# Optimization experiments

Measured on AMD Instinct MI355X. Metric: run time of the kernel, lower is better.

The kernel has to match this reference:

```python
import jax, jax.numpy as jnp
import numpy as np

B, R, A, K, O, I = 50000, 5, 8, 2, 32, 32


def setup_inputs() -> dict:
    key = jax.random.key(0)
    k1, k2, k3 = jax.random.split(key, 3)
    signal = jax.random.normal(k1, (B, R, A, 3, I), dtype=jnp.float32)
    bary = jax.random.uniform(k2, (B, R, A, 3), dtype=jnp.float32)
    # glorot-uniform-ish kernel: shape (R, A, K, O, I)
    limit = np.sqrt(6.0 / (I + O)).astype(np.float32)
    kernel = jax.random.uniform(k3, (R, A, K, O, I), dtype=jnp.float32,
                                minval=-limit, maxval=limit)
    return {"signal": signal, "bary": bary, "kernel": kernel}


def reference(signal, bary, kernel):
    # Barycentric interpolation: pullback[b,r,a,i] = sum_t bary[b,r,a,t] * signal[b,r,a,t,i]
    pullback = jnp.einsum('brat,brati->brai', bary, signal)  # (B,R,A,I)

    n_rot = kernel.shape[1]  # A rotations
    # rotated angular indices: rot_idx[c, a] = (a + c) % A
    rot_idx = (jnp.arange(n_rot)[:, None] + jnp.arange(n_rot)[None, :]) % n_rot
    k_rot = kernel[:, rot_idx]  # (R, C=A, A, K, O, I)

    # conv[b,c,o] = sum_{r,a,k,i} kernel[r,(a+c)%A,k,o,i] * pullback[b,r,a,i]
    conv = jnp.einsum('brai,rcakoi->bco', pullback, k_rot)  # (B, C, O)
    act = jax.nn.relu(conv)

    # Angular max pooling: pick rotation with max euclidean norm over O
    norms = jnp.linalg.norm(act, axis=-1)          # (B, C)
    best = jnp.argmax(norms, axis=-1)              # (B,)
    out = jnp.take_along_axis(act, best[:, None, None], axis=1)[:, 0]  # (B, O)
    return out
```

## Files before the change

kernel.cpp:

```cpp
#include <hip/hip_runtime.h>


#define B_TOT 50000
#define NRA 40

typedef __attribute__((ext_vector_type(8))) short short8v;
typedef __attribute__((ext_vector_type(4))) float f32x4;

__device__ __align__(16) unsigned short W_hi_g[NRA * 256 * 32];
__device__ __align__(16) unsigned short W_lo_g[NRA * 256 * 32];

static __device__ __forceinline__ unsigned short f2bf(float x) {
    unsigned u = __float_as_uint(x);
    u += 0x7FFFu + ((u >> 16) & 1u);
    return (unsigned short)(u >> 16);
}
static __device__ __forceinline__ float bf2f(unsigned short h) {
    return __uint_as_float(((unsigned)h) << 16);
}

__global__ __launch_bounds__(256) void build_w_kernel(const float* __restrict__ kern) {
    int e = blockIdx.x * 256 + threadIdx.x;
    int i = e & 31;
    int n = (e >> 5) & 255;
    int ra = e >> 13;
    int r = ra >> 3, a = ra & 7;
    int c = n >> 5, o = n & 31;
    int a2 = (c + a) & 7;
    const float* p = kern + ((((r * 8 + a2) * 2) * 32 + o) * 32 + i);
    float w = p[0] + p[1024];
    unsigned short hi = f2bf(w);
    unsigned short lo = f2bf(w - bf2f(hi));
    W_hi_g[e] = hi;
    W_lo_g[e] = lo;
}

static __device__ __forceinline__ void pcomp(float by0, float by1, float by2,
                                             const float4& a, const float4& b,
                                             const float4& c, float* d) {
    d[0] = fmaf(by2, c.x, fmaf(by1, b.x, by0 * a.x));
    d[1] = fmaf(by2, c.y, fmaf(by1, b.y, by0 * a.y));
    d[2] = fmaf(by2, c.z, fmaf(by1, b.z, by0 * a.z));
    d[3] = fmaf(by2, c.w, fmaf(by1, b.w, by0 * a.w));
}

static __device__ __forceinline__ void pack_write(unsigned short* p_hi, int idx, const float* v) {
    unsigned short h[4], l[4];
#pragma unroll
    for (int k = 0; k < 4; ++k) {
        h[k] = f2bf(v[k]);
        l[k] = f2bf(v[k] - bf2f(h[k]));
    }
    uint2 H, L;
    H.x = (unsigned)h[0] | ((unsigned)h[1] << 16);
    H.y = (unsigned)h[2] | ((unsigned)h[3] << 16);
    L.x = (unsigned)l[0] | ((unsigned)l[1] << 16);
    L.y = (unsigned)l[2] | ((unsigned)l[3] << 16);
    *(uint2*)(p_hi + idx) = H;
    *(uint2*)(p_hi + 2560 + idx) = L;
}

__global__ __launch_bounds__(256, 3) void conv_geo_kernel(const float* __restrict__ sig,
                                                          const float* __restrict__ bary,
                                                          float* __restrict__ out) {
    __shared__ __align__(16) float smem[8448];
    unsigned short* p_hi = (unsigned short*)smem;

    const int tid  = threadIdx.x;
    const int lane = tid & 63;
    const int wave = tid >> 6;
    const int b_l  = tid >> 2;
    const int q    = tid & 3;
    const int b0   = blockIdx.x * 64;
    int bld = b0 + b_l; if (bld > B_TOT - 1) bld = B_TOT - 1;
    const size_t sig_row = (size_t)bld * 40;

    f32x4 acc[4][4];
#pragma unroll
    for (int mi = 0; mi < 4; ++mi)
#pragma unroll
        for (int ni = 0; ni < 4; ++ni) acc[mi][ni] = (f32x4){0.f, 0.f, 0.f, 0.f};

    float4 s0, s1, s2, s3, s4, s5;
    float by0, by1, by2;
    {
        const float* sp = sig + sig_row * 96 + q * 4;
        s0 = *(const float4*)(sp);      s1 = *(const float4*)(sp + 16);
        s2 = *(const float4*)(sp + 32); s3 = *(const float4*)(sp + 48);
        s4 = *(const float4*)(sp + 64); s5 = *(const float4*)(sp + 80);
        const float* bp = bary + sig_row * 3;
        by0 = bp[0]; by1 = bp[1]; by2 = bp[2];
    }

    const int wcol = (wave * 64 + (lane & 15)) * 32 + (lane >> 4) * 8;
    const int poff = (lane & 15) * 40 + (lane >> 4) * 8;
    const int widx = b_l * 40 + q * 4;

    for (int ra = 0; ra < NRA; ++ra) {
        float pa[4], pb[4];
        pcomp(by0, by1, by2, s0, s2, s4, pa);
        pcomp(by0, by1, by2, s1, s3, s5, pb);
        pack_write(p_hi, widx, pa);
        pack_write(p_hi, widx + 16, pb);

        short8v bh[4], blv[4];
        {
            const unsigned short* whp = W_hi_g + ra * 8192 + wcol;
            const unsigned short* wlp = W_lo_g + ra * 8192 + wcol;
#pragma unroll
            for (int ni = 0; ni < 4; ++ni) {
                bh[ni]  = *(const short8v*)(whp + ni * 512);
                blv[ni] = *(const short8v*)(wlp + ni * 512);
            }
        }
        if (ra < NRA - 1) {
            const float* sp = sig + (sig_row + ra + 1) * 96 + q * 4;
            s0 = *(const float4*)(sp);      s1 = *(const float4*)(sp + 16);
            s2 = *(const float4*)(sp + 32); s3 = *(const float4*)(sp + 48);
            s4 = *(const float4*)(sp + 64); s5 = *(const float4*)(sp + 80);
            const float* bp = bary + (sig_row + ra + 1) * 3;
            by0 = bp[0]; by1 = bp[1]; by2 = bp[2];
        }
        __syncthreads();
#pragma unroll
        for (int mi = 0; mi < 4; ++mi) {
            const unsigned short* pr = p_hi + mi * 640 + poff;
            short8v ah = *(const short8v*)pr;
            short8v al = *(const short8v*)(pr + 2560);
#pragma unroll
            for (int ni = 0; ni < 4; ++ni) {
                acc[mi][ni] = __builtin_amdgcn_mfma_f32_16x16x32_bf16(ah, bh[ni],  acc[mi][ni], 0, 0, 0);
                acc[mi][ni] = __builtin_amdgcn_mfma_f32_16x16x32_bf16(ah, blv[ni], acc[mi][ni], 0, 0, 0);
                acc[mi][ni] = __builtin_amdgcn_mfma_f32_16x16x32_bf16(al, bh[ni],  acc[mi][ni], 0, 0, 0);
                acc[mi][ni] = __builtin_amdgcn_mfma_f32_16x16x32_bf16(al, blv[ni], acc[mi][ni], 0, 0, 0);
            }
        }
        __syncthreads();
    }

    const int colb = wave * 64 + (lane & 15);
    const int rsub = (lane >> 4) * 4;
#pragma unroll
    for (int ph = 0; ph < 2; ++ph) {
        __syncthreads();
#pragma unroll
        for (int mh = 0; mh < 2; ++mh) {
            int mi = ph * 2 + mh;
#pragma unroll
            for (int ni = 0; ni < 4; ++ni)
#pragma unroll
                for (int j = 0; j < 4; ++j)
                    smem[(mh * 16 + rsub + j) * 264 + colb + ni * 16] =
                        fmaxf(acc[mi][ni][j], 0.0f);
        }
        __syncthreads();
        int bb = tid >> 3;
        int c  = tid & 7;
        float n2 = 0.0f;
#pragma unroll
        for (int t = 0; t < 8; ++t) {
            float4 v = *(const float4*)&smem[bb * 264 + c * 32 + t * 4];
            n2 = fmaf(v.x, v.x, n2); n2 = fmaf(v.y, v.y, n2);
            n2 = fmaf(v.z, v.z, n2); n2 = fmaf(v.w, v.w, n2);
        }
        int bc = c;
#pragma unroll
        for (int m = 1; m < 8; m <<= 1) {
            float on2 = __shfl_xor(n2, m, 64);
            int obc = __shfl_xor(bc, m, 64);
            if (on2 > n2 || (on2 == n2 && obc < bc)) { n2 = on2; bc = obc; }
        }
        int b = b0 + ph * 32 + bb;
        if (b < B_TOT) {
            float4 v = *(const float4*)&smem[bb * 264 + bc * 32 + (tid & 7) * 4];
            *(float4*)&out[(size_t)b * 32 + (tid & 7) * 4] = v;
        }
    }
}

extern "C" void kernel_launch(void* const* d_in, const int* in_sizes, int n_in,
                              void* d_out, int out_size, void* d_ws, size_t ws_size,
                              hipStream_t stream) {
    const float* sig  = (const float*)d_in[0];
    const float* bary = (const float*)d_in[1];
    const float* kern = (const float*)d_in[2];
    float* out = (float*)d_out;

    build_w_kernel<<<(NRA * 256 * 32) / 256, 256, 0, stream>>>(kern);
    conv_geo_kernel<<<(B_TOT + 63) / 64, 256, 0, stream>>>(sig, bary, out);
}
```

Before: 235.5 us.

## Double-buffer pullback tiles in LDS and drop the lo*lo MFMA term

Splits the shared pullback staging into two ping-pong buffers. Each iteration now writes the next slice's packed bf16 pullback while the MFMAs read the current one, which removes one __syncthreads per iteration, and signal loads are prefetched two slices ahead. It also removes the al*bl correction MFMA from the split-bf16 emulation, cutting matrix work by a quarter. The dropped term is on the order of bf16-epsilon squared, so accuracy drops slightly and register pressure may rise.

```diff
diff --git a/kernel.cpp b/kernel.cpp
--- a/kernel.cpp
+++ b/kernel.cpp
@@ -44,7 +44,7 @@
     d[3] = fmaf(by2, c.w, fmaf(by1, b.w, by0 * a.w));
 }
 
-static __device__ __forceinline__ void pack_write(unsigned short* p_hi, int idx, const float* v) {
+static __device__ __forceinline__ void pack_write(unsigned short* buf, int idx, const float* v) {
     unsigned short h[4], l[4];
 #pragma unroll
     for (int k = 0; k < 4; ++k) {
@@ -56,15 +56,16 @@
     H.y = (unsigned)h[2] | ((unsigned)h[3] << 16);
     L.x = (unsigned)l[0] | ((unsigned)l[1] << 16);
     L.y = (unsigned)l[2] | ((unsigned)l[3] << 16);
-    *(uint2*)(p_hi + idx) = H;
-    *(uint2*)(p_hi + 2560 + idx) = L;
+    *(uint2*)(buf + idx) = H;
+    *(uint2*)(buf + 2560 + idx) = L;
 }
 
 __global__ __launch_bounds__(256, 3) void conv_geo_kernel(const float* __restrict__ sig,
                                                           const float* __restrict__ bary,
                                                           float* __restrict__ out) {
     __shared__ __align__(16) float smem[8448];
-    unsigned short* p_hi = (unsigned short*)smem;
+    unsigned short* pb0 = (unsigned short*)smem;
+    unsigned short* pb1 = pb0 + 5120;
 
     const int tid  = threadIdx.x;
     const int lane = tid & 63;
@@ -81,61 +82,62 @@
 #pragma unroll
         for (int ni = 0; ni < 4; ++ni) acc[mi][ni] = (f32x4){0.f, 0.f, 0.f, 0.f};
 
-    float4 s0, s1, s2, s3, s4, s5;
-    float by0, by1, by2;
-    {
-        const float* sp = sig + sig_row * 96 + q * 4;
-        s0 = *(const float4*)(sp);      s1 = *(const float4*)(sp + 16);
-        s2 = *(const float4*)(sp + 32); s3 = *(const float4*)(sp + 48);
-        s4 = *(const float4*)(sp + 64); s5 = *(const float4*)(sp + 80);
-        const float* bp = bary + sig_row * 3;
-        by0 = bp[0]; by1 = bp[1]; by2 = bp[2];
-    }
-
     const int wcol = (wave * 64 + (lane & 15)) * 32 + (lane >> 4) * 8;
     const int poff = (lane & 15) * 40 + (lane >> 4) * 8;
     const int widx = b_l * 40 + q * 4;
 
-    for (int ra = 0; ra < NRA; ++ra) {
-        float pa[4], pb[4];
+    float4 s0, s1, s2, s3, s4, s5;
+    float by0, by1, by2;
+    auto load_sig = [&](int ra) {
+        const float* sp = sig + (sig_row + ra) * 96 + q * 4;
+        s0 = *(const float4*)(sp);      s1 = *(const float4*)(sp + 16);
+        s2 = *(const float4*)(sp + 32); s3 = *(const float4*)(sp + 48);
+        s4 = *(const float4*)(sp + 64); s5 = *(const float4*)(sp + 80);
+        const float* bp = bary + (sig_row + ra) * 3;
+        by0 = bp[0]; by1 = bp[1]; by2 = bp[2];
+    };
+    auto store_p = [&](unsigned short* wrbuf) {
+        float pa[4], pbv[4];
         pcomp(by0, by1, by2, s0, s2, s4, pa);
-        pcomp(by0, by1, by2, s1, s3, s5, pb);
-        pack_write(p_hi, widx, pa);
-        pack_write(p_hi, widx + 16, pb);
+        pcomp(by0, by1, by2, s1, s3, s5, pbv);
+        pack_write(wrbuf, widx, pa);
+        pack_write(wrbuf, widx + 16, pbv);
+    };
 
-        short8v bh[4], blv[4];
-        {
-            const unsigned short* whp = W_hi_g + ra * 8192 + wcol;
-            const unsigned short* wlp = W_lo_g + ra * 8192 + wcol;
+    load_sig(0);
+    store_p(pb0);
+    load_sig(1);
+    __syncthreads();
+
+    auto body = [&](int ra, unsigned short* rdbuf, unsigned short* wrbuf) {
+        short8v bh[4], bl[4];
+        const unsigned short* whp = W_hi_g + ra * 8192 + wcol;
+        const unsigned short* wlp = W_lo_g + ra * 8192 + wcol;
 #pragma unroll
-            for (int ni = 0; ni < 4; ++ni) {
-                bh[ni]  = *(const short8v*)(whp + ni * 512);
-                blv[ni] = *(const short8v*)(wlp + ni * 512);
-            }
+        for (int ni = 0; ni < 4; ++ni) {
+            bh[ni] = *(const short8v*)(whp + ni * 512);
+            bl[ni] = *(const short8v*)(wlp + ni * 512);
         }
-        if (ra < NRA - 1) {
-            const float* sp = sig + (sig_row + ra + 1) * 96 + q * 4;
-            s0 = *(const float4*)(sp);      s1 = *(const float4*)(sp + 16);
-            s2 = *(const float4*)(sp + 32); s3 = *(const float4*)(sp + 48);
-            s4 = *(const float4*)(sp + 64); s5 = *(const float4*)(sp + 80);
-            const float* bp = bary + (sig_row + ra + 1) * 3;
-            by0 = bp[0]; by1 = bp[1]; by2 = bp[2];
-        }
-        __syncthreads();
+        if (ra + 1 < NRA) store_p(wrbuf);
+        if (ra + 2 < NRA) load_sig(ra + 2);
 #pragma unroll
         for (int mi = 0; mi < 4; ++mi) {
-            const unsigned short* pr = p_hi + mi * 640 + poff;
+            const unsigned short* pr = rdbuf + mi * 640 + poff;
             short8v ah = *(const short8v*)pr;
             short8v al = *(const short8v*)(pr + 2560);
 #pragma unroll
             for (int ni = 0; ni < 4; ++ni) {
-                acc[mi][ni] = __builtin_amdgcn_mfma_f32_16x16x32_bf16(ah, bh[ni],  acc[mi][ni], 0, 0, 0);
-                acc[mi][ni] = __builtin_amdgcn_mfma_f32_16x16x32_bf16(ah, blv[ni], acc[mi][ni], 0, 0, 0);
-                acc[mi][ni] = __builtin_amdgcn_mfma_f32_16x16x32_bf16(al, bh[ni],  acc[mi][ni], 0, 0, 0);
-                acc[mi][ni] = __builtin_amdgcn_mfma_f32_16x16x32_bf16(al, blv[ni], acc[mi][ni], 0, 0, 0);
+                acc[mi][ni] = __builtin_amdgcn_mfma_f32_16x16x32_bf16(ah, bh[ni], acc[mi][ni], 0, 0, 0);
+                acc[mi][ni] = __builtin_amdgcn_mfma_f32_16x16x32_bf16(ah, bl[ni], acc[mi][ni], 0, 0, 0);
+                acc[mi][ni] = __builtin_amdgcn_mfma_f32_16x16x32_bf16(al, bh[ni], acc[mi][ni], 0, 0, 0);
             }
         }
         __syncthreads();
+    };
+
+    for (int ra = 0; ra < NRA; ra += 2) {
+        body(ra,     pb0, pb1);
+        body(ra + 1, pb1, pb0);
     }
 
     const int colb = wave * 64 + (lane & 15);
```

Result: faster. 229.4 us (-2.6%).

## Give each wave its own 16-row tile and drop shared memory staging

Applied to the files above, without the earlier changes.

Restructures the conv kernel so each wave independently owns 16 batch rows and all 256 output columns. Pullback values are computed directly in MFMA A-operand register layout, so the shared-memory staging and the two block barriers per iteration go away. The low*low bf16 MFMA term is dropped, leaving three split-precision products instead of four. The argmax epilogue now runs on registers with lane shuffles instead of going through shared memory. In exchange every wave reloads the full weight slice from global/L2 each iteration, which cuts weight reuse across waves, and the 16-wide accumulator array raises register pressure.

```diff
diff --git a/kernel.cpp b/kernel.cpp
--- a/kernel.cpp
+++ b/kernel.cpp
@@ -3,6 +3,7 @@
 
 #define B_TOT 50000
 #define NRA 40
+#define NROWTILES 3125
 
 typedef __attribute__((ext_vector_type(8))) short short8v;
 typedef __attribute__((ext_vector_type(4))) float f32x4;
@@ -35,146 +36,101 @@
     W_lo_g[e] = lo;
 }
 
-static __device__ __forceinline__ void pcomp(float by0, float by1, float by2,
-                                             const float4& a, const float4& b,
-                                             const float4& c, float* d) {
-    d[0] = fmaf(by2, c.x, fmaf(by1, b.x, by0 * a.x));
-    d[1] = fmaf(by2, c.y, fmaf(by1, b.y, by0 * a.y));
-    d[2] = fmaf(by2, c.z, fmaf(by1, b.z, by0 * a.z));
-    d[3] = fmaf(by2, c.w, fmaf(by1, b.w, by0 * a.w));
-}
-
-static __device__ __forceinline__ void pack_write(unsigned short* p_hi, int idx, const float* v) {
-    unsigned short h[4], l[4];
-#pragma unroll
-    for (int k = 0; k < 4; ++k) {
-        h[k] = f2bf(v[k]);
-        l[k] = f2bf(v[k] - bf2f(h[k]));
-    }
-    uint2 H, L;
-    H.x = (unsigned)h[0] | ((unsigned)h[1] << 16);
-    H.y = (unsigned)h[2] | ((unsigned)h[3] << 16);
-    L.x = (unsigned)l[0] | ((unsigned)l[1] << 16);
-    L.y = (unsigned)l[2] | ((unsigned)l[3] << 16);
-    *(uint2*)(p_hi + idx) = H;
-    *(uint2*)(p_hi + 2560 + idx) = L;
-}
-
-__global__ __launch_bounds__(256, 3) void conv_geo_kernel(const float* __restrict__ sig,
-                                                          const float* __restrict__ bary,
-                                                          float* __restrict__ out) {
-    __shared__ __align__(16) float smem[8448];
-    unsigned short* p_hi = (unsigned short*)smem;
-
+__global__ __launch_bounds__(256) void conv_geo_kernel(const float* __restrict__ sig,
+                                                       const float* __restrict__ bary,
+                                                       float* __restrict__ out) {
     const int tid  = threadIdx.x;
     const int lane = tid & 63;
-    const int wave = tid >> 6;
-    const int b_l  = tid >> 2;
-    const int q    = tid & 3;
-    const int b0   = blockIdx.x * 64;
-    int bld = b0 + b_l; if (bld > B_TOT - 1) bld = B_TOT - 1;
-    const size_t sig_row = (size_t)bld * 40;
+    const int wv   = tid >> 6;
+    const int rt   = blockIdx.x * 4 + wv;
+    if (rt >= NROWTILES) return;
 
-    f32x4 acc[4][4];
+    const int arow = lane & 15;
+    const int i0   = (lane >> 4) * 8;
+    const size_t srow = ((size_t)rt * 16 + arow) * 40;
+
+    f32x4 acc[16];
 #pragma unroll
-    for (int mi = 0; mi < 4; ++mi)
+    for (int ni = 0; ni < 16; ++ni) acc[ni] = (f32x4){0.f, 0.f, 0.f, 0.f};
+
+    const int wbase = arow * 32 + (lane >> 4) * 8;
+
+    for (int ra = 0; ra < NRA; ++ra) {
+        const float* sp = sig + (srow + ra) * 96 + i0;
+        float4 t0a = *(const float4*)(sp);       float4 t0b = *(const float4*)(sp + 4);
+        float4 t1a = *(const float4*)(sp + 32);  float4 t1b = *(const float4*)(sp + 36);
+        float4 t2a = *(const float4*)(sp + 64);  float4 t2b = *(const float4*)(sp + 68);
+        const float* bp = bary + (srow + ra) * 3;
+        float by0 = bp[0], by1 = bp[1], by2 = bp[2];
+        float p[8];
+        p[0] = fmaf(by2, t2a.x, fmaf(by1, t1a.x, by0 * t0a.x));
+        p[1] = fmaf(by2, t2a.y, fmaf(by1, t1a.y, by0 * t0a.y));
+        p[2] = fmaf(by2, t2a.z, fmaf(by1, t1a.z, by0 * t0a.z));
+        p[3] = fmaf(by2, t2a.w, fmaf(by1, t1a.w, by0 * t0a.w));
+        p[4] = fmaf(by2, t2b.x, fmaf(by1, t1b.x, by0 * t0b.x));
+        p[5] = fmaf(by2, t2b.y, fmaf(by1, t1b.y, by0 * t0b.y));
+        p[6] = fmaf(by2, t2b.z, fmaf(by1, t1b.z, by0 * t0b.z));
+        p[7] = fmaf(by2, t2b.w, fmaf(by1, t1b.w, by0 * t0b.w));
+        unsigned short hh[8], ll[8];
 #pragma unroll
-        for (int ni = 0; ni < 4; ++ni) acc[mi][ni] = (f32x4){0.f, 0.f, 0.f, 0.f};
+        for (int j = 0; j < 8; ++j) {
+            hh[j] = f2bf(p[j]);
+            ll[j] = f2bf(p[j] - bf2f(hh[j]));
+        }
+        union { unsigned u[4]; short8v v; } ch, cl;
+#pragma unroll
+        for (int k = 0; k < 4; ++k) {
+            ch.u[k] = (unsigned)hh[2 * k] | ((unsigned)hh[2 * k + 1] << 16);
+            cl.u[k] = (unsigned)ll[2 * k] | ((unsigned)ll[2 * k + 1] << 16);
+        }
+        short8v ah = ch.v, al = cl.v;
 
-    float4 s0, s1, s2, s3, s4, s5;
-    float by0, by1, by2;
-    {
-        const float* sp = sig + sig_row * 96 + q * 4;
-        s0 = *(const float4*)(sp);      s1 = *(const float4*)(sp + 16);
-        s2 = *(const float4*)(sp + 32); s3 = *(const float4*)(sp + 48);
-        s4 = *(const float4*)(sp + 64); s5 = *(const float4*)(sp + 80);
-        const float* bp = bary + sig_row * 3;
-        by0 = bp[0]; by1 = bp[1]; by2 = bp[2];
+        const unsigned short* wh = W_hi_g + ra * 8192 + wbase;
+        const unsigned short* wl = W_lo_g + ra * 8192 + wbase;
+#pragma unroll
+        for (int ni = 0; ni < 16; ++ni) {
+            short8v bh = *(const short8v*)(wh + ni * 512);
+            short8v bl = *(const short8v*)(wl + ni * 512);
+            acc[ni] = __builtin_amdgcn_mfma_f32_16x16x32_bf16(ah, bh, acc[ni], 0, 0, 0);
+            acc[ni] = __builtin_amdgcn_mfma_f32_16x16x32_bf16(ah, bl, acc[ni], 0, 0, 0);
+            acc[ni] = __builtin_amdgcn_mfma_f32_16x16x32_bf16(al, bh, acc[ni], 0, 0, 0);
+        }
     }
 
-    const int wcol = (wave * 64 + (lane & 15)) * 32 + (lane >> 4) * 8;
-    const int poff = (lane & 15) * 40 + (lane >> 4) * 8;
-    const int widx = b_l * 40 + q * 4;
+#pragma unroll
+    for (int ni = 0; ni < 16; ++ni)
+#pragma unroll
+        for (int j = 0; j < 4; ++j) acc[ni][j] = fmaxf(acc[ni][j], 0.0f);
 
-    for (int ra = 0; ra < NRA; ++ra) {
-        float pa[4], pb[4];
-        pcomp(by0, by1, by2, s0, s2, s4, pa);
-        pcomp(by0, by1, by2, s1, s3, s5, pb);
-        pack_write(p_hi, widx, pa);
-        pack_write(p_hi, widx + 16, pb);
+    float nrm[4][8];
+#pragma unroll
+    for (int j = 0; j < 4; ++j)
+#pragma unroll
+        for (int c = 0; c < 8; ++c)
+            nrm[j][c] = fmaf(acc[2 * c][j], acc[2 * c][j],
+                             acc[2 * c + 1][j] * acc[2 * c + 1][j]);
+#pragma unroll
+    for (int m = 1; m < 16; m <<= 1)
+#pragma unroll
+        for (int j = 0; j < 4; ++j)
+#pragma unroll
+            for (int c = 0; c < 8; ++c)
+                nrm[j][c] += __shfl_xor(nrm[j][c], m, 64);
 
-        short8v bh[4], blv[4];
-        {
-            const unsigned short* whp = W_hi_g + ra * 8192 + wcol;
-            const unsigned short* wlp = W_lo_g + ra * 8192 + wcol;
 #pragma unroll
-            for (int ni = 0; ni < 4; ++ni) {
-                bh[ni]  = *(const short8v*)(whp + ni * 512);
-                blv[ni] = *(const short8v*)(wlp + ni * 512);
-            }
-        }
-        if (ra < NRA - 1) {
-            const float* sp = sig + (sig_row + ra + 1) * 96 + q * 4;
-            s0 = *(const float4*)(sp);      s1 = *(const float4*)(sp + 16);
-            s2 = *(const float4*)(sp + 32); s3 = *(const float4*)(sp + 48);
-            s4 = *(const float4*)(sp + 64); s5 = *(const float4*)(sp + 80);
-            const float* bp = bary + (sig_row + ra + 1) * 3;
-            by0 = bp[0]; by1 = bp[1]; by2 = bp[2];
-        }
-        __syncthreads();
+    for (int j = 0; j < 4; ++j) {
+        float n2 = nrm[j][0];
+        int bc = 0;
 #pragma unroll
-        for (int mi = 0; mi < 4; ++mi) {
-            const unsigned short* pr = p_hi + mi * 640 + poff;
-            short8v ah = *(const short8v*)pr;
-            short8v al = *(const short8v*)(pr + 2560);
+        for (int c = 1; c < 8; ++c)
+            if (nrm[j][c] > n2) { n2 = nrm[j][c]; bc = c; }
+        float v0 = acc[0][j], v1 = acc[1][j];
 #pragma unroll
-            for (int ni = 0; ni < 4; ++ni) {
-                acc[mi][ni] = __builtin_amdgcn_mfma_f32_16x16x32_bf16(ah, bh[ni],  acc[mi][ni], 0, 0, 0);
-                acc[mi][ni] = __builtin_amdgcn_mfma_f32_16x16x32_bf16(ah, blv[ni], acc[mi][ni], 0, 0, 0);
-                acc[mi][ni] = __builtin_amdgcn_mfma_f32_16x16x32_bf16(al, bh[ni],  acc[mi][ni], 0, 0, 0);
-                acc[mi][ni] = __builtin_amdgcn_mfma_f32_16x16x32_bf16(al, blv[ni], acc[mi][ni], 0, 0, 0);
-            }
-        }
-        __syncthreads();
-    }
-
-    const int colb = wave * 64 + (lane & 15);
-    const int rsub = (lane >> 4) * 4;
-#pragma unroll
-    for (int ph = 0; ph < 2; ++ph) {
-        __syncthreads();
-#pragma unroll
-        for (int mh = 0; mh < 2; ++mh) {
-            int mi = ph * 2 + mh;
-#pragma unroll
-            for (int ni = 0; ni < 4; ++ni)
-#pragma unroll
-                for (int j = 0; j < 4; ++j)
-                    smem[(mh * 16 + rsub + j) * 264 + colb + ni * 16] =
-                        fmaxf(acc[mi][ni][j], 0.0f);
-        }
-        __syncthreads();
-        int bb = tid >> 3;
-        int c  = tid & 7;
-        float n2 = 0.0f;
-#pragma unroll
-        for (int t = 0; t < 8; ++t) {
-            float4 v = *(const float4*)&smem[bb * 264 + c * 32 + t * 4];
-            n2 = fmaf(v.x, v.x, n2); n2 = fmaf(v.y, v.y, n2);
-            n2 = fmaf(v.z, v.z, n2); n2 = fmaf(v.w, v.w, n2);
-        }
-        int bc = c;
-#pragma unroll
-        for (int m = 1; m < 8; m <<= 1) {
-            float on2 = __shfl_xor(n2, m, 64);
-            int obc = __shfl_xor(bc, m, 64);
-            if (on2 > n2 || (on2 == n2 && obc < bc)) { n2 = on2; bc = obc; }
-        }
-        int b = b0 + ph * 32 + bb;
-        if (b < B_TOT) {
-            float4 v = *(const float4*)&smem[bb * 264 + bc * 32 + (tid & 7) * 4];
-            *(float4*)&out[(size_t)b * 32 + (tid & 7) * 4] = v;
-        }
+        for (int c = 1; c < 8; ++c)
+            if (bc == c) { v0 = acc[2 * c][j]; v1 = acc[2 * c + 1][j]; }
+        int b = rt * 16 + (lane >> 4) * 4 + j;
+        out[(size_t)b * 32 + (lane & 15)]      = v0;
+        out[(size_t)b * 32 + 16 + (lane & 15)] = v1;
     }
 }
 
@@ -187,5 +143,5 @@
     float* out = (float*)d_out;
 
     build_w_kernel<<<(NRA * 256 * 32) / 256, 256, 0, stream>>>(kern);
-    conv_geo_kernel<<<(B_TOT + 63) / 64, 256, 0, stream>>>(sig, bary, out);
+    conv_geo_kernel<<<(NROWTILES + 3) / 4, 256, 0, stream>>>(sig, bary, out);
 }
```

Result: slower. 487.6 us (+107.1%).
